# Kernel optimization log

Hardware: AMD Instinct MI355X
Metric: run time of the kernel (lower is better)

Reference implementation:

```python
import jax, jax.numpy as jnp
import numpy as np

B, S, IN, H, OUT = 4096, 32, 256, 128, 256


def setup_inputs() -> dict:
    key = jax.random.key(0)
    k = jax.random.split(key, 5)
    x = jax.random.normal(k[0], (B, S, IN), dtype=jnp.float32)
    # Stacked per-subband weights: torch nn.Linear computes x @ W.T + b;
    # here we store W already transposed as [S, in, out].
    W1 = jax.random.normal(k[1], (S, IN, H), dtype=jnp.float32) * (1.0 / np.sqrt(IN))
    b1 = jax.random.normal(k[2], (S, H), dtype=jnp.float32) * 0.01
    W2 = jax.random.normal(k[3], (S, H, OUT), dtype=jnp.float32) * (1.0 / np.sqrt(H))
    b2 = jax.random.normal(k[4], (S, OUT), dtype=jnp.float32) * 0.01
    return {"x": x, "W1": W1, "b1": b1, "W2": W2, "b2": b2}


def reference(x, W1, b1, W2, b2):
    # All subbands fused into one batched GEMM + ReLU + batched GEMM.
    # h: [B, S, H]
    h = jax.nn.relu(jnp.einsum('bsi,sih->bsh', x, W1) + b1)
    # out: [B, S, OUT]
    out = jnp.einsum('bsh,sho->bso', h, W2) + b2
    return out
```

## Files before the change

kernel.cpp:

```cpp
#include <hip/hip_runtime.h>
#include <hip/hip_bf16.h>

#define B_   4096
#define S_   32
#define IN_  256
#define H_   128
#define OUT_ 256

typedef __attribute__((ext_vector_type(8))) short bf16x8;
typedef __attribute__((ext_vector_type(4))) float f32x4;
typedef unsigned long long ull;

__device__ __forceinline__ unsigned short f2bf(float f) {
    union { float f; unsigned u; } v; v.f = f;
    unsigned r = v.u + 0x7FFFu + ((v.u >> 16) & 1u);
    return (unsigned short)(r >> 16);
}
__device__ __forceinline__ unsigned cvt_pk(float lo, float hi) {
    unsigned r;
    asm("v_cvt_pk_bf16_f32 %0, %1, %2" : "=v"(r) : "v"(lo), "v"(hi));
    return r;
}

__global__ __launch_bounds__(256) void pack_both(const float* __restrict__ W1,
                                                 const float* __restrict__ W2,
                                                 unsigned short* __restrict__ w1f,
                                                 unsigned short* __restrict__ w2f) {
    __shared__ float tile[32][257];
    const int bid = blockIdx.x;
    const int t = threadIdx.x;
    if (bid < 256) {
        const int s = bid >> 3, kk = bid & 7;
#pragma unroll
        for (int i = 0; i < 16; ++i) {
            int idx = t + i * 256;
            int kl = idx >> 7, h = idx & 127;
            tile[kl][h] = W1[((size_t)s * IN_ + kk * 32 + kl) * H_ + h];
        }
        __syncthreads();
#pragma unroll
        for (int rep = 0; rep < 2; ++rep) {
            int idx = t + rep * 256;
            int hf = idx >> 6, l = idx & 63, l15 = l & 15, l4 = l >> 4;
            unsigned short o8[8];
#pragma unroll
            for (int j = 0; j < 8; ++j) o8[j] = f2bf(tile[l4 * 8 + j][hf * 16 + l15]);
            *(bf16x8*)(w1f + (((size_t)(s * 8 + kk) * 8 + hf) * 64 + l) * 8) = *(bf16x8*)o8;
        }
    } else {
        const int rel = bid - 256, s = rel >> 2, kkh = rel & 3;
#pragma unroll
        for (int i = 0; i < 32; ++i) {
            int idx = t + i * 256;
            int kl = idx >> 8, o = idx & 255;
            tile[kl][o] = W2[((size_t)s * H_ + kkh * 32 + kl) * OUT_ + o];
        }
        __syncthreads();
#pragma unroll
        for (int rep = 0; rep < 4; ++rep) {
            int idx = t + rep * 256;
            int g = idx >> 6, l = idx & 63, l15 = l & 15, l4 = l >> 4;
            unsigned short o8[8];
#pragma unroll
            for (int j = 0; j < 8; ++j) o8[j] = f2bf(tile[l4 * 8 + j][g * 16 + l15]);
            *(bf16x8*)(w2f + (((size_t)(s * 16 + g) * 4 + kkh) * 64 + l) * 8) = *(bf16x8*)o8;
        }
    }
}

__global__ __launch_bounds__(512) void subband_fused_kernel(
        const float* __restrict__ x,
        const unsigned short* __restrict__ w1f,
        const unsigned short* __restrict__ w2f,
        const float* __restrict__ b1,
        const float* __restrict__ b2,
        float* __restrict__ out) {
    __shared__ __align__(16) unsigned char lds[161280];
    unsigned char* w1l = lds;
    unsigned char* w2l = lds + 65536;
    unsigned char* repb = lds + 126976;
    float* b1l = (float*)(lds + 159744);
    float* b2l = (float*)(lds + 160256);

    const int bid = blockIdx.x;
    const int s     = bid >> 3;
    const int chunk = bid & 7;
    const int tid = threadIdx.x;
    const int w = tid >> 6, l = tid & 63, l15 = l & 15, l4 = l >> 4;
    unsigned char* rep = repb + w * 4096;
    const int rw = chunk * 512 + w * 64;

#define LDG(dst, p) asm volatile("global_load_dwordx4 %0, %1, off" : "=v"(dst) : "v"(p))

    f32x4 v[16];
    {
        const float* xr = x + ((size_t)(rw + l15) * S_ + s) * IN_ + l4 * 8;
#pragma unroll
        for (int kk = 0; kk < 8; ++kk) {
            LDG(v[2 * kk],     xr + kk * 32);
            LDG(v[2 * kk + 1], xr + kk * 32 + 4);
        }
    }

    const unsigned char* w1src = (const unsigned char*)(w1f + (size_t)s * 32768);
#pragma unroll
    for (int i = 0; i < 8; ++i)
        *(bf16x8*)(w1l + tid * 16 + i * 8192) = *(const bf16x8*)(w1src + tid * 16 + i * 8192);
    const unsigned char* w2src = (const unsigned char*)(w2f + (size_t)s * 32768);
#pragma unroll
    for (int i = 0; i < 7; ++i)
        *(bf16x8*)(w2l + tid * 16 + i * 8192) = *(const bf16x8*)(w2src + tid * 16 + i * 8192);
    if (tid < 256)
        *(bf16x8*)(w2l + tid * 16 + 57344) = *(const bf16x8*)(w2src + tid * 16 + 57344);

    bf16x8 w2r[4];
#pragma unroll
    for (int kkh = 0; kkh < 4; ++kkh)
        w2r[kkh] = *(const bf16x8*)(w2src + (((size_t)15 * 4 + kkh) * 64 + l) * 16);

    if (tid < 128)      b1l[tid]       = b1[s * H_ + tid];
    else if (tid < 384) b2l[tid - 128] = b2[s * OUT_ + (tid - 128)];

    __syncthreads();

    float* opbase = out + ((size_t)(rw + l15) * S_ + s) * OUT_;

#pragma unroll 1
    for (int t = 0; t < 4; ++t) {
        asm volatile("s_waitcnt vmcnt(0)"
            : "+v"(v[0]), "+v"(v[1]), "+v"(v[2]), "+v"(v[3]),
              "+v"(v[4]), "+v"(v[5]), "+v"(v[6]), "+v"(v[7]),
              "+v"(v[8]), "+v"(v[9]), "+v"(v[10]), "+v"(v[11]),
              "+v"(v[12]), "+v"(v[13]), "+v"(v[14]), "+v"(v[15]) :: "memory");
        __builtin_amdgcn_sched_barrier(0);

        bf16x8 xb[8];
#pragma unroll
        for (int kk = 0; kk < 8; ++kk) {
            union { unsigned u[4]; bf16x8 b; } p;
            p.u[0] = cvt_pk(v[2 * kk][0],     v[2 * kk][1]);
            p.u[1] = cvt_pk(v[2 * kk][2],     v[2 * kk][3]);
            p.u[2] = cvt_pk(v[2 * kk + 1][0], v[2 * kk + 1][1]);
            p.u[3] = cvt_pk(v[2 * kk + 1][2], v[2 * kk + 1][3]);
            xb[kk] = p.b;
        }

        if (t < 3) {
            const float* xr = x + ((size_t)(rw + (t + 1) * 16 + l15) * S_ + s) * IN_ + l4 * 8;
#pragma unroll
            for (int kk = 0; kk < 8; ++kk) {
                LDG(v[2 * kk],     xr + kk * 32);
                LDG(v[2 * kk + 1], xr + kk * 32 + 4);
            }
        }

        f32x4 acc1[8];
#pragma unroll
        for (int hf = 0; hf < 8; ++hf) {
            const float4 bv = *(const float4*)(b1l + hf * 16 + l4 * 4);
            acc1[hf][0] = bv.x; acc1[hf][1] = bv.y; acc1[hf][2] = bv.z; acc1[hf][3] = bv.w;
        }
        __builtin_amdgcn_s_setprio(1);
#pragma unroll
        for (int kk = 0; kk < 8; ++kk)
#pragma unroll
            for (int hf = 0; hf < 8; ++hf) {
                const bf16x8 wf = *(const bf16x8*)(w1l + ((kk * 8 + hf) * 64 + l) * 16);
                acc1[hf] = __builtin_amdgcn_mfma_f32_16x16x32_bf16(wf, xb[kk], acc1[hf], 0, 0, 0);
            }
        __builtin_amdgcn_s_setprio(0);

#pragma unroll
        for (int hf = 0; hf < 8; ++hf) {
            unsigned p0 = cvt_pk(fmaxf(acc1[hf][0], 0.f), fmaxf(acc1[hf][1], 0.f));
            unsigned p1 = cvt_pk(fmaxf(acc1[hf][2], 0.f), fmaxf(acc1[hf][3], 0.f));
            ull p = (ull)p0 | ((ull)p1 << 32);
            const int kkh = hf >> 1;
            const int l4p = ((hf & 1) << 1) | (l4 >> 1);
            *(ull*)(rep + kkh * 1024 + (l4p * 16 + l15) * 16 + ((l4 & 1) * 8)) = p;
        }
        asm volatile("s_waitcnt lgkmcnt(0)" ::: "memory");
        __builtin_amdgcn_sched_barrier(0);

        bf16x8 hfr[4];
#pragma unroll
        for (int kkh = 0; kkh < 4; ++kkh)
            hfr[kkh] = *(const bf16x8*)(rep + kkh * 1024 + l * 16);

        float* op = opbase + (size_t)t * 16 * S_ * OUT_;
#pragma unroll
        for (int g = 0; g < 16; ++g) {
            const float4 bv = *(const float4*)(b2l + g * 16 + l4 * 4);
            f32x4 acc2;
            acc2[0] = bv.x; acc2[1] = bv.y; acc2[2] = bv.z; acc2[3] = bv.w;
            __builtin_amdgcn_s_setprio(1);
#pragma unroll
            for (int kkh = 0; kkh < 4; ++kkh) {
                const bf16x8 wf = (g < 15)
                    ? *(const bf16x8*)(w2l + ((g * 4 + kkh) * 64 + l) * 16)
                    : w2r[kkh];
                acc2 = __builtin_amdgcn_mfma_f32_16x16x32_bf16(wf, hfr[kkh], acc2, 0, 0, 0);
            }
            __builtin_amdgcn_s_setprio(0);
            *(f32x4*)(op + g * 16 + l4 * 4) = acc2;
        }
    }
#undef LDG
}

extern "C" void kernel_launch(void* const* d_in, const int* in_sizes, int n_in,
                              void* d_out, int out_size, void* d_ws, size_t ws_size,
                              hipStream_t stream) {
    const float* x  = (const float*)d_in[0];
    const float* W1 = (const float*)d_in[1];
    const float* b1 = (const float*)d_in[2];
    const float* W2 = (const float*)d_in[3];
    const float* b2 = (const float*)d_in[4];
    float* out = (float*)d_out;

    unsigned short* w1f = (unsigned short*)d_ws;
    unsigned short* w2f = w1f + (size_t)S_ * 8 * 8 * 64 * 8;

    pack_both<<<384, 256, 0, stream>>>(W1, W2, w1f, w2f);
    subband_fused_kernel<<<256, 512, 0, stream>>>(x, w1f, w2f, b1, b2, out);
}
```

Baseline: 70.73 us.

## Process two 16-row tiles per iteration to reuse LDS weight fragments

Restructures the per-wave loop to handle two 16-row x tiles together, so each W1 and W2 fragment read from LDS feeds two MFMAs. This halves LDS weight traffic per output and interleaves independent MFMA chains. The cost is more live registers for the doubled accumulators, and weaker x prefetch overlap. The second tile's load is now awaited right after it is issued, before any compute.

```diff
diff --git a/kernel.cpp b/kernel.cpp
--- a/kernel.cpp
+++ b/kernel.cpp
@@ -91,16 +91,55 @@
     const int rw = chunk * 512 + w * 64;
 
 #define LDG(dst, p) asm volatile("global_load_dwordx4 %0, %1, off" : "=v"(dst) : "v"(p))
+#define WAITV0                                                                   \
+    asm volatile("s_waitcnt vmcnt(0)"                                            \
+        : "+v"(v[0]), "+v"(v[1]), "+v"(v[2]), "+v"(v[3]),                        \
+          "+v"(v[4]), "+v"(v[5]), "+v"(v[6]), "+v"(v[7]),                        \
+          "+v"(v[8]), "+v"(v[9]), "+v"(v[10]), "+v"(v[11]),                      \
+          "+v"(v[12]), "+v"(v[13]), "+v"(v[14]), "+v"(v[15]) :: "memory")
+#define ISSUE_X(ROW0)                                                            \
+    do {                                                                         \
+        const float* xr_ = x + ((size_t)((ROW0) + l15) * S_ + s) * IN_ + l4 * 8; \
+        _Pragma("unroll")                                                        \
+        for (int kk = 0; kk < 8; ++kk) {                                         \
+            LDG(v[2 * kk],     xr_ + kk * 32);                                   \
+            LDG(v[2 * kk + 1], xr_ + kk * 32 + 4);                               \
+        }                                                                        \
+    } while (0)
+#define CVT_XB(XB)                                                               \
+    do {                                                                         \
+        _Pragma("unroll")                                                        \
+        for (int kk = 0; kk < 8; ++kk) {                                         \
+            union { unsigned u[4]; bf16x8 b; } p;                                \
+            p.u[0] = cvt_pk(v[2 * kk][0],     v[2 * kk][1]);                     \
+            p.u[1] = cvt_pk(v[2 * kk][2],     v[2 * kk][3]);                     \
+            p.u[2] = cvt_pk(v[2 * kk + 1][0], v[2 * kk + 1][1]);                 \
+            p.u[3] = cvt_pk(v[2 * kk + 1][2], v[2 * kk + 1][3]);                 \
+            XB[kk] = p.b;                                                        \
+        }                                                                        \
+    } while (0)
+#define REPACK(ACC, HFR)                                                         \
+    do {                                                                         \
+        _Pragma("unroll")                                                        \
+        for (int hf = 0; hf < 8; ++hf) {                                         \
+            unsigned p0 = cvt_pk(fmaxf(ACC[hf][0], 0.f), fmaxf(ACC[hf][1], 0.f));\
+            unsigned p1 = cvt_pk(fmaxf(ACC[hf][2], 0.f), fmaxf(ACC[hf][3], 0.f));\
+            ull p = (ull)p0 | ((ull)p1 << 32);                                   \
+            const int kkh = hf >> 1;                                             \
+            const int l4p = ((hf & 1) << 1) | (l4 >> 1);                         \
+            *(ull*)(rep + kkh * 1024 + (l4p * 16 + l15) * 16 + ((l4 & 1) * 8)) = p; \
+        }                                                                        \
+        asm volatile("s_waitcnt lgkmcnt(0)" ::: "memory");                       \
+        __builtin_amdgcn_sched_barrier(0);                                       \
+        _Pragma("unroll")                                                        \
+        for (int kkh = 0; kkh < 4; ++kkh)                                        \
+            HFR[kkh] = *(const bf16x8*)(rep + kkh * 1024 + l * 16);              \
+        asm volatile("s_waitcnt lgkmcnt(0)" ::: "memory");                       \
+        __builtin_amdgcn_sched_barrier(0);                                       \
+    } while (0)
 
     f32x4 v[16];
-    {
-        const float* xr = x + ((size_t)(rw + l15) * S_ + s) * IN_ + l4 * 8;
-#pragma unroll
-        for (int kk = 0; kk < 8; ++kk) {
-            LDG(v[2 * kk],     xr + kk * 32);
-            LDG(v[2 * kk + 1], xr + kk * 32 + 4);
-        }
-    }
+    ISSUE_X(rw);
 
     const unsigned char* w1src = (const unsigned char*)(w1f + (size_t)s * 32768);
 #pragma unroll
@@ -125,86 +164,71 @@
 
     float* opbase = out + ((size_t)(rw + l15) * S_ + s) * OUT_;
 
-#pragma unroll 1
-    for (int t = 0; t < 4; ++t) {
-        asm volatile("s_waitcnt vmcnt(0)"
-            : "+v"(v[0]), "+v"(v[1]), "+v"(v[2]), "+v"(v[3]),
-              "+v"(v[4]), "+v"(v[5]), "+v"(v[6]), "+v"(v[7]),
-              "+v"(v[8]), "+v"(v[9]), "+v"(v[10]), "+v"(v[11]),
-              "+v"(v[12]), "+v"(v[13]), "+v"(v[14]), "+v"(v[15]) :: "memory");
-        __builtin_amdgcn_sched_barrier(0);
-
-        bf16x8 xb[8];
-#pragma unroll
-        for (int kk = 0; kk < 8; ++kk) {
-            union { unsigned u[4]; bf16x8 b; } p;
-            p.u[0] = cvt_pk(v[2 * kk][0],     v[2 * kk][1]);
-            p.u[1] = cvt_pk(v[2 * kk][2],     v[2 * kk][3]);
-            p.u[2] = cvt_pk(v[2 * kk + 1][0], v[2 * kk + 1][1]);
-            p.u[3] = cvt_pk(v[2 * kk + 1][2], v[2 * kk + 1][3]);
-            xb[kk] = p.b;
-        }
-
-        if (t < 3) {
-            const float* xr = x + ((size_t)(rw + (t + 1) * 16 + l15) * S_ + s) * IN_ + l4 * 8;
-#pragma unroll
-            for (int kk = 0; kk < 8; ++kk) {
-                LDG(v[2 * kk],     xr + kk * 32);
-                LDG(v[2 * kk + 1], xr + kk * 32 + 4);
-            }
-        }
-
-        f32x4 acc1[8];
-#pragma unroll
-        for (int hf = 0; hf < 8; ++hf) {
-            const float4 bv = *(const float4*)(b1l + hf * 16 + l4 * 4);
-            acc1[hf][0] = bv.x; acc1[hf][1] = bv.y; acc1[hf][2] = bv.z; acc1[hf][3] = bv.w;
-        }
-        __builtin_amdgcn_s_setprio(1);
-#pragma unroll
-        for (int kk = 0; kk < 8; ++kk)
-#pragma unroll
-            for (int hf = 0; hf < 8; ++hf) {
-                const bf16x8 wf = *(const bf16x8*)(w1l + ((kk * 8 + hf) * 64 + l) * 16);
-                acc1[hf] = __builtin_amdgcn_mfma_f32_16x16x32_bf16(wf, xb[kk], acc1[hf], 0, 0, 0);
-            }
-        __builtin_amdgcn_s_setprio(0);
-
-#pragma unroll
-        for (int hf = 0; hf < 8; ++hf) {
-            unsigned p0 = cvt_pk(fmaxf(acc1[hf][0], 0.f), fmaxf(acc1[hf][1], 0.f));
-            unsigned p1 = cvt_pk(fmaxf(acc1[hf][2], 0.f), fmaxf(acc1[hf][3], 0.f));
-            ull p = (ull)p0 | ((ull)p1 << 32);
-            const int kkh = hf >> 1;
-            const int l4p = ((hf & 1) << 1) | (l4 >> 1);
-            *(ull*)(rep + kkh * 1024 + (l4p * 16 + l15) * 16 + ((l4 & 1) * 8)) = p;
-        }
-        asm volatile("s_waitcnt lgkmcnt(0)" ::: "memory");
-        __builtin_amdgcn_sched_barrier(0);
-
-        bf16x8 hfr[4];
-#pragma unroll
-        for (int kkh = 0; kkh < 4; ++kkh)
-            hfr[kkh] = *(const bf16x8*)(rep + kkh * 1024 + l * 16);
-
-        float* op = opbase + (size_t)t * 16 * S_ * OUT_;
-#pragma unroll
-        for (int g = 0; g < 16; ++g) {
-            const float4 bv = *(const float4*)(b2l + g * 16 + l4 * 4);
-            f32x4 acc2;
-            acc2[0] = bv.x; acc2[1] = bv.y; acc2[2] = bv.z; acc2[3] = bv.w;
-            __builtin_amdgcn_s_setprio(1);
-#pragma unroll
-            for (int kkh = 0; kkh < 4; ++kkh) {
-                const bf16x8 wf = (g < 15)
-                    ? *(const bf16x8*)(w2l + ((g * 4 + kkh) * 64 + l) * 16)
-                    : w2r[kkh];
-                acc2 = __builtin_amdgcn_mfma_f32_16x16x32_bf16(wf, hfr[kkh], acc2, 0, 0, 0);
-            }
-            __builtin_amdgcn_s_setprio(0);
-            *(f32x4*)(op + g * 16 + l4 * 4) = acc2;
-        }
-    }
+#define PAIR_BODY(T, DO_NEXT)                                                    \
+do {                                                                             \
+    WAITV0;                                                                      \
+    __builtin_amdgcn_sched_barrier(0);                                           \
+    bf16x8 xbA[8], xbB[8];                                                       \
+    CVT_XB(xbA);                                                                 \
+    ISSUE_X(rw + ((T) + 1) * 16);                                                \
+    WAITV0;                                                                      \
+    __builtin_amdgcn_sched_barrier(0);                                           \
+    CVT_XB(xbB);                                                                 \
+    f32x4 acc1A[8], acc1B[8];                                                    \
+    _Pragma("unroll")                                                            \
+    for (int hf = 0; hf < 8; ++hf) {                                             \
+        const float4 bv = *(const float4*)(b1l + hf * 16 + l4 * 4);              \
+        acc1A[hf][0] = bv.x; acc1A[hf][1] = bv.y;                                \
+        acc1A[hf][2] = bv.z; acc1A[hf][3] = bv.w;                                \
+        acc1B[hf] = acc1A[hf];                                                   \
+    }                                                                            \
+    __builtin_amdgcn_s_setprio(1);                                               \
+    _Pragma("unroll")                                                            \
+    for (int kk = 0; kk < 8; ++kk)                                               \
+        _Pragma("unroll")                                                        \
+        for (int hf = 0; hf < 8; ++hf) {                                         \
+            const bf16x8 wf = *(const bf16x8*)(w1l + ((kk * 8 + hf) * 64 + l) * 16); \
+            acc1A[hf] = __builtin_amdgcn_mfma_f32_16x16x32_bf16(                 \
+                wf, xbA[kk], acc1A[hf], 0, 0, 0);                                \
+            acc1B[hf] = __builtin_amdgcn_mfma_f32_16x16x32_bf16(                 \
+                wf, xbB[kk], acc1B[hf], 0, 0, 0);                                \
+        }                                                                        \
+    __builtin_amdgcn_s_setprio(0);                                               \
+    bf16x8 hfrA[4], hfrB[4];                                                     \
+    REPACK(acc1A, hfrA);                                                         \
+    REPACK(acc1B, hfrB);                                                         \
+    if (DO_NEXT) ISSUE_X(rw + ((T) + 2) * 16);                                   \
+    float* opA = opbase + (size_t)(T) * 16 * S_ * OUT_;                          \
+    float* opB = opA + (size_t)16 * S_ * OUT_;                                   \
+    _Pragma("unroll")                                                            \
+    for (int g = 0; g < 16; ++g) {                                               \
+        const float4 bv = *(const float4*)(b2l + g * 16 + l4 * 4);               \
+        f32x4 accA, accB;                                                        \
+        accA[0] = bv.x; accA[1] = bv.y; accA[2] = bv.z; accA[3] = bv.w;          \
+        accB = accA;                                                             \
+        __builtin_amdgcn_s_setprio(1);                                           \
+        _Pragma("unroll")                                                        \
+        for (int kkh = 0; kkh < 4; ++kkh) {                                      \
+            const bf16x8 wf = (g < 15)                                           \
+                ? *(const bf16x8*)(w2l + ((g * 4 + kkh) * 64 + l) * 16)          \
+                : w2r[kkh];                                                      \
+            accA = __builtin_amdgcn_mfma_f32_16x16x32_bf16(wf, hfrA[kkh], accA, 0, 0, 0); \
+            accB = __builtin_amdgcn_mfma_f32_16x16x32_bf16(wf, hfrB[kkh], accB, 0, 0, 0); \
+        }                                                                        \
+        __builtin_amdgcn_s_setprio(0);                                           \
+        *(f32x4*)(opA + g * 16 + l4 * 4) = accA;                                 \
+        *(f32x4*)(opB + g * 16 + l4 * 4) = accB;                                 \
+    }                                                                            \
+} while (0)
+
+    PAIR_BODY(0, 1);
+    PAIR_BODY(2, 0);
+
+#undef PAIR_BODY
+#undef REPACK
+#undef CVT_XB
+#undef ISSUE_X
+#undef WAITV0
 #undef LDG
 }
 
```

Result: faster. 67.58 us (median of 2 runs) (-4.4%).

## Use 12 waves per block with round-robin row tiles and split repack

Applied to the files above, without the earlier changes.

Raises the block size from 8 to 12 waves. Row tiles are now assigned round-robin across waves instead of a fixed 4 tiles per wave, with the x prefetch following the next assigned tile. The per-wave LDS repack buffer is halved, so the ReLU-to-bf16 transpose is done in two halves with extra waits. The intent is more latency hiding per CU. The costs are load imbalance (some waves get 2 tiles, others 3), extra LDS synchronisation, and a much tighter register budget per thread at 768 threads that may cause spills.

```diff
diff --git a/kernel.cpp b/kernel.cpp
--- a/kernel.cpp
+++ b/kernel.cpp
@@ -68,7 +68,7 @@
     }
 }
 
-__global__ __launch_bounds__(512) void subband_fused_kernel(
+__global__ __launch_bounds__(768) void subband_fused_kernel(
         const float* __restrict__ x,
         const unsigned short* __restrict__ w1f,
         const unsigned short* __restrict__ w2f,
@@ -87,31 +87,38 @@
     const int chunk = bid & 7;
     const int tid = threadIdx.x;
     const int w = tid >> 6, l = tid & 63, l15 = l & 15, l4 = l >> 4;
-    unsigned char* rep = repb + w * 4096;
-    const int rw = chunk * 512 + w * 64;
+    unsigned char* rep = repb + w * 2048;
 
 #define LDG(dst, p) asm volatile("global_load_dwordx4 %0, %1, off" : "=v"(dst) : "v"(p))
+#define WAITV0                                                                   \
+    asm volatile("s_waitcnt vmcnt(0)"                                            \
+        : "+v"(v[0]), "+v"(v[1]), "+v"(v[2]), "+v"(v[3]),                        \
+          "+v"(v[4]), "+v"(v[5]), "+v"(v[6]), "+v"(v[7]),                        \
+          "+v"(v[8]), "+v"(v[9]), "+v"(v[10]), "+v"(v[11]),                      \
+          "+v"(v[12]), "+v"(v[13]), "+v"(v[14]), "+v"(v[15]) :: "memory")
+#define ISSUE_X(ROW0)                                                            \
+    do {                                                                         \
+        const float* xr_ = x + ((size_t)((ROW0) + l15) * S_ + s) * IN_ + l4 * 8; \
+        _Pragma("unroll")                                                        \
+        for (int kk = 0; kk < 8; ++kk) {                                         \
+            LDG(v[2 * kk],     xr_ + kk * 32);                                   \
+            LDG(v[2 * kk + 1], xr_ + kk * 32 + 4);                               \
+        }                                                                        \
+    } while (0)
 
     f32x4 v[16];
-    {
-        const float* xr = x + ((size_t)(rw + l15) * S_ + s) * IN_ + l4 * 8;
-#pragma unroll
-        for (int kk = 0; kk < 8; ++kk) {
-            LDG(v[2 * kk],     xr + kk * 32);
-            LDG(v[2 * kk + 1], xr + kk * 32 + 4);
-        }
-    }
+    ISSUE_X(chunk * 512 + w * 16);
 
     const unsigned char* w1src = (const unsigned char*)(w1f + (size_t)s * 32768);
 #pragma unroll
-    for (int i = 0; i < 8; ++i)
-        *(bf16x8*)(w1l + tid * 16 + i * 8192) = *(const bf16x8*)(w1src + tid * 16 + i * 8192);
+    for (int i = 0; i < 5; ++i)
+        *(bf16x8*)(w1l + tid * 16 + i * 12288) = *(const bf16x8*)(w1src + tid * 16 + i * 12288);
+    if (tid < 256)
+        *(bf16x8*)(w1l + tid * 16 + 61440) = *(const bf16x8*)(w1src + tid * 16 + 61440);
     const unsigned char* w2src = (const unsigned char*)(w2f + (size_t)s * 32768);
 #pragma unroll
-    for (int i = 0; i < 7; ++i)
-        *(bf16x8*)(w2l + tid * 16 + i * 8192) = *(const bf16x8*)(w2src + tid * 16 + i * 8192);
-    if (tid < 256)
-        *(bf16x8*)(w2l + tid * 16 + 57344) = *(const bf16x8*)(w2src + tid * 16 + 57344);
+    for (int i = 0; i < 5; ++i)
+        *(bf16x8*)(w2l + tid * 16 + i * 12288) = *(const bf16x8*)(w2src + tid * 16 + i * 12288);
 
     bf16x8 w2r[4];
 #pragma unroll
@@ -123,15 +130,13 @@
 
     __syncthreads();
 
-    float* opbase = out + ((size_t)(rw + l15) * S_ + s) * OUT_;
-
 #pragma unroll 1
-    for (int t = 0; t < 4; ++t) {
-        asm volatile("s_waitcnt vmcnt(0)"
-            : "+v"(v[0]), "+v"(v[1]), "+v"(v[2]), "+v"(v[3]),
-              "+v"(v[4]), "+v"(v[5]), "+v"(v[6]), "+v"(v[7]),
-              "+v"(v[8]), "+v"(v[9]), "+v"(v[10]), "+v"(v[11]),
-              "+v"(v[12]), "+v"(v[13]), "+v"(v[14]), "+v"(v[15]) :: "memory");
+    for (int r = 0; r < 3; ++r) {
+        const int tile = r * 12 + w;
+        if (tile >= 32) continue;
+        const int rowt = chunk * 512 + tile * 16;
+
+        WAITV0;
         __builtin_amdgcn_sched_barrier(0);
 
         bf16x8 xb[8];
@@ -145,13 +150,9 @@
             xb[kk] = p.b;
         }
 
-        if (t < 3) {
-            const float* xr = x + ((size_t)(rw + (t + 1) * 16 + l15) * S_ + s) * IN_ + l4 * 8;
-#pragma unroll
-            for (int kk = 0; kk < 8; ++kk) {
-                LDG(v[2 * kk],     xr + kk * 32);
-                LDG(v[2 * kk + 1], xr + kk * 32 + 4);
-            }
+        {
+            const int ntile = (r + 1) * 12 + w;
+            if (r < 2 && ntile < 32) ISSUE_X(chunk * 512 + ntile * 16);
         }
 
         f32x4 acc1[8];
@@ -170,24 +171,28 @@
             }
         __builtin_amdgcn_s_setprio(0);
 
-#pragma unroll
-        for (int hf = 0; hf < 8; ++hf) {
-            unsigned p0 = cvt_pk(fmaxf(acc1[hf][0], 0.f), fmaxf(acc1[hf][1], 0.f));
-            unsigned p1 = cvt_pk(fmaxf(acc1[hf][2], 0.f), fmaxf(acc1[hf][3], 0.f));
-            ull p = (ull)p0 | ((ull)p1 << 32);
-            const int kkh = hf >> 1;
-            const int l4p = ((hf & 1) << 1) | (l4 >> 1);
-            *(ull*)(rep + kkh * 1024 + (l4p * 16 + l15) * 16 + ((l4 & 1) * 8)) = p;
-        }
-        asm volatile("s_waitcnt lgkmcnt(0)" ::: "memory");
-        __builtin_amdgcn_sched_barrier(0);
-
         bf16x8 hfr[4];
 #pragma unroll
-        for (int kkh = 0; kkh < 4; ++kkh)
-            hfr[kkh] = *(const bf16x8*)(rep + kkh * 1024 + l * 16);
-
-        float* op = opbase + (size_t)t * 16 * S_ * OUT_;
+        for (int half = 0; half < 2; ++half) {
+#pragma unroll
+            for (int hh = 0; hh < 4; ++hh) {
+                const int hf = half * 4 + hh;
+                unsigned p0 = cvt_pk(fmaxf(acc1[hf][0], 0.f), fmaxf(acc1[hf][1], 0.f));
+                unsigned p1 = cvt_pk(fmaxf(acc1[hf][2], 0.f), fmaxf(acc1[hf][3], 0.f));
+                ull p = (ull)p0 | ((ull)p1 << 32);
+                const int loc = (hf >> 1) & 1;
+                const int l4p = ((hf & 1) << 1) | (l4 >> 1);
+                *(ull*)(rep + loc * 1024 + (l4p * 16 + l15) * 16 + ((l4 & 1) * 8)) = p;
+            }
+            asm volatile("s_waitcnt lgkmcnt(0)" ::: "memory");
+            __builtin_amdgcn_sched_barrier(0);
+            hfr[half * 2 + 0] = *(const bf16x8*)(rep + l * 16);
+            hfr[half * 2 + 1] = *(const bf16x8*)(rep + 1024 + l * 16);
+            asm volatile("s_waitcnt lgkmcnt(0)" ::: "memory");
+            __builtin_amdgcn_sched_barrier(0);
+        }
+
+        float* op = out + ((size_t)(rowt + l15) * S_ + s) * OUT_;
 #pragma unroll
         for (int g = 0; g < 16; ++g) {
             const float4 bv = *(const float4*)(b2l + g * 16 + l4 * 4);
@@ -205,6 +210,8 @@
             *(f32x4*)(op + g * 16 + l4 * 4) = acc2;
         }
     }
+#undef ISSUE_X
+#undef WAITV0
 #undef LDG
 }
 
@@ -222,5 +229,5 @@
     unsigned short* w2f = w1f + (size_t)S_ * 8 * 8 * 64 * 8;
 
     pack_both<<<384, 256, 0, stream>>>(W1, W2, w1f, w2f);
-    subband_fused_kernel<<<256, 512, 0, stream>>>(x, w1f, w2f, b1, b2, out);
-}
+    subband_fused_kernel<<<256, 768, 0, stream>>>(x, w1f, w2f, b1, b2, out);
+}
```

New measurement: 68.23 us. 1.04x faster.
